# Kernel tuning notes

Measured on AMD Instinct MI355X. Metric: run time of the kernel, lower is better.

Reference implementation:

```python
import jax, jax.numpy as jnp
import numpy as np

V, E, S, NCLASS = 50000, 512, 1024, 2
B, L = 64, 256


def setup_inputs() -> dict:
    key = jax.random.key(0)
    ks = jax.random.split(key, 8)
    inputs = jax.random.randint(ks[0], (B, L), 0, V)
    emb_table = jax.random.normal(ks[1], (V, E), dtype=jnp.float32) * 0.02
    Wc = jax.random.normal(ks[2], (S, 2 * E), dtype=jnp.float32) * (1.0 / np.sqrt(2 * E))
    bc = jnp.zeros((S,), dtype=jnp.float32)
    W1 = jax.random.normal(ks[3], (50, S), dtype=jnp.float32) * (1.0 / np.sqrt(S))
    b1 = jnp.zeros((50,), dtype=jnp.float32)
    W2 = jax.random.normal(ks[4], (NCLASS, 50), dtype=jnp.float32) * (1.0 / np.sqrt(50))
    b2 = jnp.zeros((NCLASS,), dtype=jnp.float32)
    return {"inputs": inputs, "emb_table": emb_table, "Wc": Wc, "bc": bc,
            "W1": W1, "b1": b1, "W2": W2, "b2": b2}


def reference(inputs, emb_table, Wc, bc, W1, b1, W2, b2):
    # [B, L, E] embedding lookup
    w_embs = emb_table[inputs]
    # sliding-window pair concat: [B, L-1, 2E]
    pairs = jnp.concatenate([w_embs[:, :-1, :], w_embs[:, 1:, :]], axis=-1)
    # conv linear: [B, L-1, S]
    conv = jnp.einsum('blf,sf->bls', pairs, Wc) + bc
    # max-pool over positions then sigmoid: [B, S]
    sent = jax.nn.sigmoid(jnp.max(conv, axis=1))
    # classifier: S -> 50 -> NCLASS
    h = jnp.einsum('bs,hs->bh', sent, W1) + b1
    logits = jnp.einsum('bh,ch->bc', h, W2) + b2
    out = jax.nn.log_softmax(logits, axis=1)
    return jnp.squeeze(out, axis=1) if out.shape[1] == 1 else out
```

## Files before the change

### kernel.cpp

```cpp
#include <hip/hip_runtime.h>

#define VV 50000
#define EE 512
#define SS 1024
#define BB 64
#define LL 256
#define NTOK (BB*LL)
#define XROWS_PAD (NTOK + 8)

#define SCALE_A 0x79797979
#define SCALE_B 0x7A7A7A7A

typedef __attribute__((ext_vector_type(8))) int i32x8;
typedef __attribute__((ext_vector_type(4))) float f32x4;

static __device__ __forceinline__ void glds16(const void* g, void* l) {
    __builtin_amdgcn_global_load_lds(
        (const __attribute__((address_space(1))) unsigned int*)g,
        (__attribute__((address_space(3))) unsigned int*)l,
        16, 0, 0);
}

static __device__ __forceinline__ uint2 pack8_fp8(float4 v0, float4 v1, float s) {
    int r0 = __builtin_amdgcn_cvt_pk_fp8_f32(v0.x * s, v0.y * s, 0, 0);
    r0 = __builtin_amdgcn_cvt_pk_fp8_f32(v0.z * s, v0.w * s, r0, 1);
    int r1 = __builtin_amdgcn_cvt_pk_fp8_f32(v1.x * s, v1.y * s, 0, 0);
    r1 = __builtin_amdgcn_cvt_pk_fp8_f32(v1.z * s, v1.w * s, r1, 1);
    uint2 o; o.x = (unsigned)r0; o.y = (unsigned)r1; return o;
}

static __device__ __forceinline__ i32x8 ldfrag(const unsigned char* rowbase, int c0, int c1) {
    const uint4 lo = *(const uint4*)(rowbase + c0 * 16);
    const uint4 hi = *(const uint4*)(rowbase + c1 * 16);
    i32x8 f;
    f[0] = lo.x; f[1] = lo.y; f[2] = lo.z; f[3] = lo.w;
    f[4] = hi.x; f[5] = hi.y; f[6] = hi.z; f[7] = hi.w;
    return f;
}

__global__ void gather_fp8_kernel(const int* __restrict__ inputs,
                                  const float* __restrict__ emb,
                                  unsigned char* __restrict__ Xq) {
    const int t = blockIdx.x;
    const int idx = inputs[t];
    const int lane = threadIdx.x;
    const float4 v0 = *(const float4*)(emb + (size_t)idx * EE + lane * 8);
    const float4 v1 = *(const float4*)(emb + (size_t)idx * EE + lane * 8 + 4);
    *(uint2*)(Xq + (size_t)t * EE + lane * 8) = pack8_fp8(v0, v1, 64.0f);
}

__global__ void wc_fp8_kernel(const float* __restrict__ Wc,
                              unsigned char* __restrict__ Wq,
                              unsigned int* __restrict__ pre) {
    const int i = (blockIdx.x * 256 + threadIdx.x) * 8;
    const float4 v0 = *(const float4*)(Wc + i);
    const float4 v1 = *(const float4*)(Wc + i + 4);
    *(uint2*)(Wq + i) = pack8_fp8(v0, v1, 32.0f);
    if (blockIdx.x < BB) {
        uint4 z = {0u, 0u, 0u, 0u};
        *(uint4*)(pre + blockIdx.x * SS + threadIdx.x * 4) = z;
    }
}

__global__ __launch_bounds__(256, 3)
void conv_gemm_kernel(const unsigned char* __restrict__ Xq,
                      const unsigned char* __restrict__ Wq,
                      unsigned int* __restrict__ pre) {
    __shared__ unsigned char sX[136 * 128];
    __shared__ unsigned char sW[256 * 128];

    const int tid = threadIdx.x;
    const int w = tid >> 6;
    const int lane = tid & 63;
    const int wx = w & 1;
    const int wy = w >> 1;
    const int m0 = blockIdx.y * 128;
    const int s0 = blockIdx.x * 128;

    f32x4 acc[4][4];
    #pragma unroll
    for (int mt = 0; mt < 4; ++mt)
        #pragma unroll
        for (int nt = 0; nt < 4; ++nt)
            acc[mt][nt] = (f32x4){0.f, 0.f, 0.f, 0.f};

    const int lrow = lane >> 3;
    const int lcolsw = (((lane & 7) ^ lrow) * 16);
    const int quad = lane >> 4;
    const int l15 = lane & 15;
    const int swA  = l15 & 7;
    const int swA1 = (l15 + 1) & 7;
    const int cb0 = 2 * quad;

    for (int kt = 0; kt < 4; ++kt) {
        const int k0 = kt * 128;
        #pragma unroll
        for (int i = 0; i < 4; ++i) {
            const int c = w + 4 * i;
            glds16(Xq + (size_t)(m0 + c * 8 + lrow) * EE + k0 + lcolsw,
                   (char*)sX + c * 1024);
        }
        if (w == 0) {
            glds16(Xq + (size_t)(m0 + 128 + lrow) * EE + k0 + lcolsw,
                   (char*)sX + 16 * 1024);
        }
        #pragma unroll
        for (int i = 0; i < 8; ++i) {
            const int c = w + 4 * i;
            const int wrow = c * 8 + lrow;
            const int h = wrow >> 7, sl = wrow & 127;
            glds16(Wq + (size_t)(s0 + sl) * 1024 + h * 512 + k0 + lcolsw,
                   (char*)sW + c * 1024);
        }
        __syncthreads();

        #pragma unroll
        for (int mg = 0; mg < 2; ++mg) {
            i32x8 aA[2], aB[2];
            #pragma unroll
            for (int j = 0; j < 2; ++j) {
                const int r = wy * 64 + (mg * 2 + j) * 16 + l15;
                aA[j] = ldfrag(sX + r * 128, cb0 ^ swA, (cb0 + 1) ^ swA);
                aB[j] = ldfrag(sX + (r + 1) * 128, cb0 ^ swA1, (cb0 + 1) ^ swA1);
            }
            #pragma unroll
            for (int nt = 0; nt < 4; ++nt) {
                const int rB = wx * 64 + nt * 16 + l15;
                const i32x8 b1 = ldfrag(sW + rB * 128, cb0 ^ swA, (cb0 + 1) ^ swA);
                const i32x8 b2 = ldfrag(sW + (128 + rB) * 128, cb0 ^ swA, (cb0 + 1) ^ swA);
                #pragma unroll
                for (int j = 0; j < 2; ++j) {
                    const int mt = mg * 2 + j;
                    acc[mt][nt] = __builtin_amdgcn_mfma_scale_f32_16x16x128_f8f6f4(
                        aA[j], b1, acc[mt][nt], 0, 0, 0, SCALE_A, 0, SCALE_B);
                    acc[mt][nt] = __builtin_amdgcn_mfma_scale_f32_16x16x128_f8f6f4(
                        aB[j], b2, acc[mt][nt], 0, 0, 0, SCALE_A, 0, SCALE_B);
                }
            }
        }
        __syncthreads();
    }

    const int b = m0 >> 8;
    float* smax = (float*)sX;
    #pragma unroll
    for (int nt = 0; nt < 4; ++nt) {
        float cmax = -3.4e38f;
        #pragma unroll
        for (int mt = 0; mt < 4; ++mt) {
            const int rbase = m0 + wy * 64 + mt * 16 + quad * 4;
            #pragma unroll
            for (int r = 0; r < 4; ++r) {
                const float v = acc[mt][nt][r];
                const bool valid = (((rbase + r) & 255) != 255);
                cmax = valid ? fmaxf(cmax, v) : cmax;
            }
        }
        cmax = fmaxf(cmax, __shfl_xor(cmax, 16));
        cmax = fmaxf(cmax, __shfl_xor(cmax, 32));
        if (lane < 16) smax[wy * 128 + wx * 64 + nt * 16 + lane] = cmax;
    }
    __syncthreads();
    if (tid < 128) {
        const float m = fmaxf(smax[tid], smax[128 + tid]);
        const unsigned int u = __float_as_uint(m);
        const unsigned int e = (u & 0x80000000u) ? ~u : (u | 0x80000000u);
        atomicMax(pre + b * SS + s0 + tid, e);
    }
}

__global__ __launch_bounds__(1024)
void classifier_kernel(const unsigned int* __restrict__ pre,
                       const float* __restrict__ bc,
                       const float* __restrict__ W1,
                       const float* __restrict__ b1,
                       const float* __restrict__ W2,
                       const float* __restrict__ b2,
                       float* __restrict__ out) {
    __shared__ float ssig[SS];
    __shared__ float sh[64];
    const int b = blockIdx.x;
    const int tid = threadIdx.x;
    {
        const unsigned int e = pre[b * SS + tid];
        const unsigned int u = (e & 0x80000000u) ? (e & 0x7FFFFFFFu) : ~e;
        const float x = __uint_as_float(u) + bc[tid];
        ssig[tid] = 1.0f / (1.0f + __expf(-x));
    }
    if (tid >= 50 && tid < 64) sh[tid] = 0.f;
    __syncthreads();
    const int w = tid >> 6, lane = tid & 63;
    const float4* sp = (const float4*)ssig;
    for (int j = w; j < 50; j += 16) {
        const float4* wp = (const float4*)(W1 + j * SS);
        float p = 0.f;
        #pragma unroll
        for (int i = 0; i < 4; ++i) {
            const float4 a = sp[lane + i * 64];
            const float4 g = wp[lane + i * 64];
            p += a.x * g.x + a.y * g.y + a.z * g.z + a.w * g.w;
        }
        #pragma unroll
        for (int off = 32; off; off >>= 1) p += __shfl_xor(p, off);
        if (lane == 0) sh[j] = p + b1[j];
    }
    __syncthreads();
    if (w == 0) {
        const float hj = (lane < 50) ? sh[lane] : 0.f;
        const float w2a = (lane < 50) ? W2[lane] : 0.f;
        const float w2b = (lane < 50) ? W2[50 + lane] : 0.f;
        float l0 = hj * w2a, l1 = hj * w2b;
        #pragma unroll
        for (int off = 32; off; off >>= 1) {
            l0 += __shfl_xor(l0, off);
            l1 += __shfl_xor(l1, off);
        }
        if (lane == 0) {
            l0 += b2[0]; l1 += b2[1];
            const float m = fmaxf(l0, l1);
            const float lse = m + logf(expf(l0 - m) + expf(l1 - m));
            out[b * 2 + 0] = l0 - lse;
            out[b * 2 + 1] = l1 - lse;
        }
    }
}

extern "C" void kernel_launch(void* const* d_in, const int* in_sizes, int n_in,
                              void* d_out, int out_size, void* d_ws, size_t ws_size,
                              hipStream_t stream) {
    const int*   inputs = (const int*)  d_in[0];
    const float* emb    = (const float*)d_in[1];
    const float* Wc     = (const float*)d_in[2];
    const float* bc     = (const float*)d_in[3];
    const float* W1     = (const float*)d_in[4];
    const float* b1     = (const float*)d_in[5];
    const float* W2     = (const float*)d_in[6];
    const float* b2     = (const float*)d_in[7];
    float* out = (float*)d_out;

    unsigned char* Xq = (unsigned char*)d_ws;
    unsigned char* Wq = Xq + (size_t)XROWS_PAD * EE;
    unsigned int*  pre = (unsigned int*)(Wq + (size_t)SS * 1024);

    gather_fp8_kernel<<<NTOK, 64, 0, stream>>>(inputs, emb, Xq);
    wc_fp8_kernel<<<512, 256, 0, stream>>>(Wc, Wq, pre);
    dim3 grid(SS / 128, NTOK / 128);
    conv_gemm_kernel<<<grid, 256, 0, stream>>>(Xq, Wq, pre);
    classifier_kernel<<<BB, 1024, 0, stream>>>(pre, bc, W1, b1, W2, b2, out);
}
```

Baseline: 207.2 us.

## Fuse gather and weight quantization kernels; load all A fragments before MFMA loop

Merges the embedding-gather FP8 quantization kernel and the conv-weight quantization kernel into one launch with 256-thread blocks, where each block handles four tokens or one weight chunk. This removes one kernel launch and the small 64-thread blocks. In the GEMM inner loop, all four A and shifted-A fragments are loaded up front with precomputed LDS base pointers, and the MFMAs are reordered so the B fragments are loaded once per tile. The cost is higher register pressure, which may hurt occupancy under the 3-blocks-per-SM launch bound.

```diff
diff --git a/kernel.cpp b/kernel.cpp
--- a/kernel.cpp
+++ b/kernel.cpp
@@ -38,27 +38,32 @@
     return f;
 }
 
-__global__ void gather_fp8_kernel(const int* __restrict__ inputs,
-                                  const float* __restrict__ emb,
-                                  unsigned char* __restrict__ Xq) {
-    const int t = blockIdx.x;
-    const int idx = inputs[t];
-    const int lane = threadIdx.x;
-    const float4 v0 = *(const float4*)(emb + (size_t)idx * EE + lane * 8);
-    const float4 v1 = *(const float4*)(emb + (size_t)idx * EE + lane * 8 + 4);
-    *(uint2*)(Xq + (size_t)t * EE + lane * 8) = pack8_fp8(v0, v1, 64.0f);
-}
-
-__global__ void wc_fp8_kernel(const float* __restrict__ Wc,
-                              unsigned char* __restrict__ Wq,
-                              unsigned int* __restrict__ pre) {
-    const int i = (blockIdx.x * 256 + threadIdx.x) * 8;
-    const float4 v0 = *(const float4*)(Wc + i);
-    const float4 v1 = *(const float4*)(Wc + i + 4);
-    *(uint2*)(Wq + i) = pack8_fp8(v0, v1, 32.0f);
-    if (blockIdx.x < BB) {
-        uint4 z = {0u, 0u, 0u, 0u};
-        *(uint4*)(pre + blockIdx.x * SS + threadIdx.x * 4) = z;
+__global__ __launch_bounds__(256)
+void prep_kernel(const int* __restrict__ inputs,
+                 const float* __restrict__ emb,
+                 const float* __restrict__ Wc,
+                 unsigned char* __restrict__ Xq,
+                 unsigned char* __restrict__ Wq,
+                 unsigned int* __restrict__ pre) {
+    const int tid = threadIdx.x;
+    if (blockIdx.x < 4096) {
+        const int t = blockIdx.x * 4 + (tid >> 6);
+        const int lane = tid & 63;
+        const int idx = inputs[t];
+        const float* src = emb + (size_t)idx * EE + lane * 8;
+        const float4 v0 = *(const float4*)src;
+        const float4 v1 = *(const float4*)(src + 4);
+        *(uint2*)(Xq + (size_t)t * EE + lane * 8) = pack8_fp8(v0, v1, 64.0f);
+    } else {
+        const int bb = blockIdx.x - 4096;
+        const int i = (bb * 256 + tid) * 8;
+        const float4 v0 = *(const float4*)(Wc + i);
+        const float4 v1 = *(const float4*)(Wc + i + 4);
+        *(uint2*)(Wq + i) = pack8_fp8(v0, v1, 32.0f);
+        if (bb < BB) {
+            uint4 z = {0u, 0u, 0u, 0u};
+            *(uint4*)(pre + bb * SS + tid * 4) = z;
+        }
     }
 }
 
@@ -92,6 +97,13 @@
     const int swA1 = (l15 + 1) & 7;
     const int cb0 = 2 * quad;
 
+    const unsigned char* pA  = sX + (wy * 64 + l15) * 128;
+    const unsigned char* pA1 = sX + (wy * 64 + l15 + 1) * 128;
+    const unsigned char* pB1 = sW + (wx * 64 + l15) * 128;
+    const unsigned char* pB2 = sW + (128 + wx * 64 + l15) * 128;
+    const int cA0 = cb0 ^ swA,  cA1 = (cb0 + 1) ^ swA;
+    const int cS0 = cb0 ^ swA1, cS1 = (cb0 + 1) ^ swA1;
+
     for (int kt = 0; kt < 4; ++kt) {
         const int k0 = kt * 128;
         #pragma unroll
@@ -114,29 +126,24 @@
         }
         __syncthreads();
 
-        #pragma unroll
-        for (int mg = 0; mg < 2; ++mg) {
-            i32x8 aA[2], aB[2];
+        i32x8 aA[4], aB[4];
+        #pragma unroll
+        for (int mt = 0; mt < 4; ++mt) {
+            aA[mt] = ldfrag(pA  + mt * 2048, cA0, cA1);
+            aB[mt] = ldfrag(pA1 + mt * 2048, cS0, cS1);
+        }
+        #pragma unroll
+        for (int nt = 0; nt < 4; ++nt) {
+            const i32x8 b1 = ldfrag(pB1 + nt * 2048, cA0, cA1);
+            const i32x8 b2 = ldfrag(pB2 + nt * 2048, cA0, cA1);
             #pragma unroll
-            for (int j = 0; j < 2; ++j) {
-                const int r = wy * 64 + (mg * 2 + j) * 16 + l15;
-                aA[j] = ldfrag(sX + r * 128, cb0 ^ swA, (cb0 + 1) ^ swA);
-                aB[j] = ldfrag(sX + (r + 1) * 128, cb0 ^ swA1, (cb0 + 1) ^ swA1);
-            }
+            for (int mt = 0; mt < 4; ++mt)
+                acc[mt][nt] = __builtin_amdgcn_mfma_scale_f32_16x16x128_f8f6f4(
+                    aA[mt], b1, acc[mt][nt], 0, 0, 0, SCALE_A, 0, SCALE_B);
             #pragma unroll
-            for (int nt = 0; nt < 4; ++nt) {
-                const int rB = wx * 64 + nt * 16 + l15;
-                const i32x8 b1 = ldfrag(sW + rB * 128, cb0 ^ swA, (cb0 + 1) ^ swA);
-                const i32x8 b2 = ldfrag(sW + (128 + rB) * 128, cb0 ^ swA, (cb0 + 1) ^ swA);
-                #pragma unroll
-                for (int j = 0; j < 2; ++j) {
-                    const int mt = mg * 2 + j;
-                    acc[mt][nt] = __builtin_amdgcn_mfma_scale_f32_16x16x128_f8f6f4(
-                        aA[j], b1, acc[mt][nt], 0, 0, 0, SCALE_A, 0, SCALE_B);
-                    acc[mt][nt] = __builtin_amdgcn_mfma_scale_f32_16x16x128_f8f6f4(
-                        aB[j], b2, acc[mt][nt], 0, 0, 0, SCALE_A, 0, SCALE_B);
-                }
-            }
+            for (int mt = 0; mt < 4; ++mt)
+                acc[mt][nt] = __builtin_amdgcn_mfma_scale_f32_16x16x128_f8f6f4(
+                    aB[mt], b2, acc[mt][nt], 0, 0, 0, SCALE_A, 0, SCALE_B);
         }
         __syncthreads();
     }
@@ -242,8 +249,7 @@
     unsigned char* Wq = Xq + (size_t)XROWS_PAD * EE;
     unsigned int*  pre = (unsigned int*)(Wq + (size_t)SS * 1024);
 
-    gather_fp8_kernel<<<NTOK, 64, 0, stream>>>(inputs, emb, Xq);
-    wc_fp8_kernel<<<512, 256, 0, stream>>>(Wc, Wq, pre);
+    prep_kernel<<<4608, 256, 0, stream>>>(inputs, emb, Wc, Xq, Wq, pre);
     dim3 grid(SS / 128, NTOK / 128);
     conv_gemm_kernel<<<grid, 256, 0, stream>>>(Xq, Wq, pre);
     classifier_kernel<<<BB, 1024, 0, stream>>>(pre, bc, W1, b1, W2, b2, out);
```

Result: no change. 203.4 us (-1.8%).
